# Performance work log

Measured on AMD Instinct MI355X. Metric: run time of the kernel, lower is better.

## Reference

```python
import jax, jax.numpy as jnp
import numpy as np

N_NODES = 50000
N_EDGES = 800000
NODE_DIM = 64
EDGE_DIM = 16
NUM_LAYERS = 2


def setup_inputs() -> dict:
    key = jax.random.key(0)
    ks = jax.random.split(key, 16)
    nd, ed = NODE_DIM, EDGE_DIM
    cin = 2 * nd + ed  # 144
    s = 0.05
    return {
        "x": jax.random.normal(ks[0], (N_NODES, nd), jnp.float32),
        "edge_index": jax.random.randint(ks[1], (2, N_EDGES), 0, N_NODES, jnp.int64),
        "edge_features": jax.random.normal(ks[2], (N_EDGES, ed), jnp.float32),
        "num_nodes": N_NODES,
        # shared SAGE conv params (one conv module reused every layer)
        "conv_W": jax.random.normal(ks[3], (nd + nd + ed, nd), jnp.float32) * s,
        "conv_b": jnp.zeros((nd,), jnp.float32),
        # edge-prediction MLP head: (2*nd+ed) -> 256 -> 128 -> 64 -> 1
        "W1": jax.random.normal(ks[4], (cin, 256), jnp.float32) * s,
        "b1": jnp.zeros((256,), jnp.float32),
        "W2": jax.random.normal(ks[5], (256, 128), jnp.float32) * s,
        "b2": jnp.zeros((128,), jnp.float32),
        "W3": jax.random.normal(ks[6], (128, 64), jnp.float32) * s,
        "b3": jnp.zeros((64,), jnp.float32),
        "W4": jax.random.normal(ks[7], (64, 1), jnp.float32) * s,
        "b4": jnp.zeros((1,), jnp.float32),
    }


def _sage_conv(x, src, dst, edge_features, conv_W, conv_b, num_nodes):
    # message: concat(source node feature, edge feature), mean-aggregated at dst
    msg = jnp.concatenate([x[src], edge_features], axis=-1)  # [E, nd+ed]
    agg = jax.ops.segment_sum(msg, dst, num_segments=num_nodes)
    cnt = jax.ops.segment_sum(jnp.ones((src.shape[0],), x.dtype), dst, num_segments=num_nodes)
    agg = agg / jnp.maximum(cnt, 1.0)[:, None]
    h = jnp.concatenate([x, agg], axis=-1)  # [N, 2*nd+ed]
    return h @ conv_W + conv_b  # [N, nd]


def reference(x, edge_index, edge_features, num_nodes,
              conv_W, conv_b, W1, b1, W2, b2, W3, b3, W4, b4):
    src = edge_index[0]
    dst = edge_index[1]
    h = x
    for _ in range(NUM_LAYERS):
        h = _sage_conv(h, src, dst, edge_features, conv_W, conv_b, num_nodes)
        h = jax.nn.relu(h)  # dropout is identity in eval mode
    # edge prediction head: gather endpoint embeddings + edge features -> MLP
    pair = jnp.concatenate([h[src], h[dst], edge_features], axis=-1)  # [E, 2*nd+ed]
    z = jax.nn.relu(pair @ W1 + b1)
    z = jax.nn.relu(z @ W2 + b2)
    z = jax.nn.relu(z @ W3 + b3)
    return z @ W4 + b4  # [E, 1]
```

## Files before the change

### kernel.cpp

```cpp
#include <hip/hip_runtime.h>

#define ND 64
#define ED 16
#define NN 50000
#define NE 800000
#define CIN 144
#define AGGD 80
#define TE 32

typedef __attribute__((ext_vector_type(8))) short short8;
typedef __attribute__((ext_vector_type(4))) float f32x4;
typedef __attribute__((ext_vector_type(4))) unsigned int uint4v;
typedef __attribute__((ext_vector_type(4))) unsigned short ushort4v;

union FragU { uint4v u; short8 s; };

__device__ __forceinline__ unsigned bf16rne(float v) {
  unsigned u = __float_as_uint(v);
  return (u + 0x7fffu + ((u >> 16) & 1u)) >> 16;
}


__global__ __launch_bounds__(256) void count_kernel(const int* __restrict__ dst,
                                                    int* __restrict__ dcnt) {
  int t = blockIdx.x * 256 + threadIdx.x;
  if (t < NE) atomicAdd(&dcnt[dst[t]], 1);
}

__global__ __launch_bounds__(1024) void scan_kernel(const int* __restrict__ dcnt,
                                                    int* __restrict__ base) {
  __shared__ int s[1024];
  __shared__ int carry;
  int t = threadIdx.x;
  if (t == 0) carry = 0;
  __syncthreads();
  for (int c = 0; c < (NN + 1023) / 1024; ++c) {
    int i = c * 1024 + t;
    int v = (i < NN) ? dcnt[i] : 0;
    s[t] = v;
    __syncthreads();
    #pragma unroll
    for (int d = 1; d < 1024; d <<= 1) {
      int add = (t >= d) ? s[t - d] : 0;
      __syncthreads();
      s[t] += add;
      __syncthreads();
    }
    if (i < NN) base[i] = carry + s[t] - v;
    int tot = s[1023];
    __syncthreads();
    if (t == 0) carry += tot;
    __syncthreads();
  }
}

__global__ __launch_bounds__(256) void place_kernel(const int* __restrict__ src,
                                                    const int* __restrict__ dst,
                                                    const int* __restrict__ base,
                                                    int* __restrict__ fill,
                                                    int* __restrict__ sidx,
                                                    int* __restrict__ eidx) {
  int e = blockIdx.x * 256 + threadIdx.x;
  if (e < NE) {
    int d = dst[e];
    int slot = base[d] + atomicAdd(&fill[d], 1);
    sidx[slot] = src[e];
    eidx[slot] = e;
  }
}

template<bool WITH_EF>
__global__ __launch_bounds__(256) void gather_kernel(const float* __restrict__ h,
                                                     const int* __restrict__ sidx,
                                                     const int* __restrict__ eidx,
                                                     const float* __restrict__ ef,
                                                     const int* __restrict__ base,
                                                     const int* __restrict__ dcnt,
                                                     float* __restrict__ agg) {
  int wid  = (blockIdx.x * 256 + threadIdx.x) >> 6;
  int lane = threadIdx.x & 63;
  if (wid >= NN) return;
  int b0 = base[wid], deg = dcnt[wid];
  float acc = 0.f;
  int k = 0;
  for (; k + 2 <= deg; k += 2) {
    int s0 = sidx[b0 + k], s1 = sidx[b0 + k + 1];
    float a = h[(size_t)s0 * ND + lane];
    float b = h[(size_t)s1 * ND + lane];
    acc += a + b;
  }
  if (k < deg) acc += h[(size_t)sidx[b0 + k] * ND + lane];
  agg[(size_t)wid * AGGD + lane] = acc;
  if (WITH_EF) {
    int sub = lane >> 4, f = lane & 15;
    float ae = 0.f;
    for (int kk = sub; kk < deg; kk += 4)
      ae += ef[(size_t)eidx[b0 + kk] * ED + f];
    ae += __shfl_down(ae, 32);
    ae += __shfl_down(ae, 16);
    if (lane < 16) agg[(size_t)wid * AGGD + ND + lane] = ae;
  }
}

__global__ __launch_bounds__(256) void node_kernel(const float* __restrict__ h,
                                                   const float* __restrict__ agg,
                                                   const int* __restrict__ dcnt,
                                                   const float* __restrict__ W,
                                                   const float* __restrict__ b,
                                                   float* __restrict__ hout) {
  __shared__ float in[4][CIN];
  int j  = threadIdx.x & 63;
  int nl = threadIdx.x >> 6;
  int n  = blockIdx.x * 4 + nl;
  float inv = 1.0f / fmaxf((float)dcnt[n], 1.0f);
  in[nl][j]      = h[(size_t)n * ND + j];
  in[nl][ND + j] = agg[(size_t)n * AGGD + j] * inv;
  if (j < ED) in[nl][2 * ND + j] = agg[(size_t)n * AGGD + ND + j] * inv;
  __syncthreads();
  float acc = b[j];
  #pragma unroll 4
  for (int i = 0; i < CIN; i++)
    acc = fmaf(in[nl][i], W[i * ND + j], acc);
  hout[(size_t)n * ND + j] = fmaxf(acc, 0.0f);
}

template<int K, int KP, int NO, bool LO>
__global__ __launch_bounds__(256) void prep_kernel(const float* __restrict__ W,
                                                   unsigned short* __restrict__ WT) {
  constexpr int KS = KP / 32;
  int idx = blockIdx.x * 256 + threadIdx.x;
  if (idx >= KP * NO) return;
  int i  = idx & 7;
  int lr = (idx >> 3) & 15;
  int lk = (idx >> 7) & 3;
  int rest = idx >> 9;
  int ks = rest % KS, ct = rest / KS;
  int k = ks * 32 + lk * 8 + i;
  int n = ct * 16 + lr;
  float wv = (k < K) ? W[k * NO + n] : 0.f;
  unsigned hi = bf16rne(wv);
  unsigned outb = hi;
  if (LO) {
    float lo = wv - __uint_as_float(hi << 16);
    outb = bf16rne(lo);
  }
  WT[idx] = (unsigned short)outb;
}

template<int KP, int NO, int SIN, int SOUT, int CTW, bool F32OUT>
__device__ __forceinline__ void mfma_layer(
    const unsigned short* __restrict__ zh, const unsigned short* __restrict__ zl,
    unsigned short* __restrict__ oh, unsigned short* __restrict__ ol,
    float* __restrict__ of,
    const unsigned short* __restrict__ WTh, const unsigned short* __restrict__ WTl,
    const float* __restrict__ bias, int w, int l) {
  constexpr int KS = KP / 32;
  const int lr = l & 15, lk = l >> 4;
  const int ct0 = w * CTW;
  const unsigned short* a0h = zh + lr * SIN + lk * 8;
  const unsigned short* a1h = a0h + 16 * SIN;
  const unsigned short* a0l = zl + lr * SIN + lk * 8;
  const unsigned short* a1l = a0l + 16 * SIN;
  const unsigned short* wth = WTh + (size_t)(ct0 * KS) * 512 + l * 8;
  const unsigned short* wtl = WTl + (size_t)(ct0 * KS) * 512 + l * 8;

  f32x4 acc[CTW][2];
  #pragma unroll
  for (int j = 0; j < CTW; ++j) {
    acc[j][0] = f32x4{0.f, 0.f, 0.f, 0.f};
    acc[j][1] = f32x4{0.f, 0.f, 0.f, 0.f};
  }

  FragU whf[CTW], wlf[CTW], nwh[CTW], nwl[CTW];
  #pragma unroll
  for (int j = 0; j < CTW; ++j) {
    whf[j].u = *(const uint4v*)(wth + j * KS * 512);
    wlf[j].u = *(const uint4v*)(wtl + j * KS * 512);
  }

  #pragma unroll
  for (int ks = 0; ks < KS; ++ks) {
    FragU A0h, A1h, A0l, A1l;
    A0h.s = *(const short8*)(a0h + ks * 32);
    A1h.s = *(const short8*)(a1h + ks * 32);
    A0l.s = *(const short8*)(a0l + ks * 32);
    A1l.s = *(const short8*)(a1l + ks * 32);
    if (ks + 1 < KS) {
      #pragma unroll
      for (int j = 0; j < CTW; ++j) {
        nwh[j].u = *(const uint4v*)(wth + (j * KS + ks + 1) * 512);
        nwl[j].u = *(const uint4v*)(wtl + (j * KS + ks + 1) * 512);
      }
    }
    #pragma unroll
    for (int j = 0; j < CTW; ++j) {
      acc[j][0] = __builtin_amdgcn_mfma_f32_16x16x32_bf16(A0h.s, whf[j].s, acc[j][0], 0, 0, 0);
      acc[j][1] = __builtin_amdgcn_mfma_f32_16x16x32_bf16(A1h.s, whf[j].s, acc[j][1], 0, 0, 0);
      acc[j][0] = __builtin_amdgcn_mfma_f32_16x16x32_bf16(A0l.s, whf[j].s, acc[j][0], 0, 0, 0);
      acc[j][1] = __builtin_amdgcn_mfma_f32_16x16x32_bf16(A1l.s, whf[j].s, acc[j][1], 0, 0, 0);
      acc[j][0] = __builtin_amdgcn_mfma_f32_16x16x32_bf16(A0h.s, wlf[j].s, acc[j][0], 0, 0, 0);
      acc[j][1] = __builtin_amdgcn_mfma_f32_16x16x32_bf16(A1h.s, wlf[j].s, acc[j][1], 0, 0, 0);
    }
    if (ks + 1 < KS) {
      #pragma unroll
      for (int j = 0; j < CTW; ++j) { whf[j] = nwh[j]; wlf[j] = nwl[j]; }
    }
  }

  #pragma unroll
  for (int j = 0; j < CTW; ++j) {
    const int col = (ct0 + j) * 16 + lr;
    const float bb = bias[col];
    #pragma unroll
    for (int rb = 0; rb < 2; ++rb) {
      #pragma unroll
      for (int q = 0; q < 4; ++q) {
        const int row = rb * 16 + lk * 4 + q;
        float v = fmaxf(acc[j][rb][q] + bb, 0.f);
        if (F32OUT) {
          of[row * SOUT + col] = v;
        } else {
          unsigned hu = bf16rne(v);
          oh[row * SOUT + col] = (unsigned short)hu;
          float lo = v - __uint_as_float(hu << 16);
          ol[row * SOUT + col] = (unsigned short)bf16rne(lo);
        }
      }
    }
  }
}

__global__ __launch_bounds__(256, 2) void head_kernel(
    const float* __restrict__ h,
    const int* __restrict__ src, const int* __restrict__ dst,
    const float* __restrict__ ef,
    const unsigned short* __restrict__ WTh1, const unsigned short* __restrict__ WTl1,
    const unsigned short* __restrict__ WTh2, const unsigned short* __restrict__ WTl2,
    const unsigned short* __restrict__ WTh3, const unsigned short* __restrict__ WTl3,
    const float* __restrict__ b1, const float* __restrict__ b2,
    const float* __restrict__ b3,
    const float* __restrict__ W4, const float* __restrict__ b4,
    float* __restrict__ out) {
  __shared__ __align__(16) unsigned short bufA[2 * 32 * 168];
  __shared__ __align__(16) unsigned short bufB[2 * 32 * 264];
  const int t = threadIdx.x;
  const int e0 = blockIdx.x * TE;
  const int w = t >> 6, l = t & 63;

  unsigned short* PH  = bufA;
  unsigned short* PL  = bufA + 32 * 168;
  unsigned short* Z1H = bufB;
  unsigned short* Z1L = bufB + 32 * 264;
  unsigned short* Z2H = bufA;
  unsigned short* Z2L = bufA + 32 * 136;
  float* Z3 = (float*)bufB;

  {
    int el = t & 31, q = t >> 5;
    int e = e0 + el;
    int s = src[e], d = dst[e];
    #pragma unroll
    for (int p5 = 0; p5 < 5; ++p5) {
      int qq = q + p5 * 8;
      float4 v = {0.f, 0.f, 0.f, 0.f};
      if (qq < 16)      v = ((const float4*)(h + (size_t)s * ND))[qq];
      else if (qq < 32) v = ((const float4*)(h + (size_t)d * ND))[qq - 16];
      else if (qq < 36) v = ((const float4*)(ef + (size_t)e * ED))[qq - 32];
      unsigned h0 = bf16rne(v.x), h1 = bf16rne(v.y),
               h2 = bf16rne(v.z), h3 = bf16rne(v.w);
      ushort4v hv = {(unsigned short)h0, (unsigned short)h1,
                     (unsigned short)h2, (unsigned short)h3};
      ushort4v lv = {(unsigned short)bf16rne(v.x - __uint_as_float(h0 << 16)),
                     (unsigned short)bf16rne(v.y - __uint_as_float(h1 << 16)),
                     (unsigned short)bf16rne(v.z - __uint_as_float(h2 << 16)),
                     (unsigned short)bf16rne(v.w - __uint_as_float(h3 << 16))};
      *(ushort4v*)(PH + el * 168 + qq * 4) = hv;
      *(ushort4v*)(PL + el * 168 + qq * 4) = lv;
    }
  }
  __syncthreads();
  mfma_layer<160, 256, 168, 264, 4, false>(PH, PL, Z1H, Z1L, nullptr,
                                           WTh1, WTl1, b1, w, l);
  __syncthreads();
  mfma_layer<256, 128, 264, 136, 2, false>(Z1H, Z1L, Z2H, Z2L, nullptr,
                                           WTh2, WTl2, b2, w, l);
  __syncthreads();
  mfma_layer<128, 64, 136, 68, 1, true>(Z2H, Z2L, nullptr, nullptr, Z3,
                                        WTh3, WTl3, b3, w, l);
  __syncthreads();
  if (t < TE) {
    const float* zr = Z3 + t * 68;
    float acc = b4[0];
    #pragma unroll
    for (int q = 0; q < 16; ++q) {
      float4 z  = *(const float4*)(zr + q * 4);
      float4 wv = *(const float4*)(W4 + q * 4);
      acc = fmaf(z.x, wv.x, acc); acc = fmaf(z.y, wv.y, acc);
      acc = fmaf(z.z, wv.z, acc); acc = fmaf(z.w, wv.w, acc);
    }
    out[e0 + t] = acc;
  }
}


extern "C" void kernel_launch(void* const* d_in, const int* in_sizes, int n_in,
                              void* d_out, int out_size, void* d_ws, size_t ws_size,
                              hipStream_t stream) {
  const float* x  = (const float*)d_in[0];
  const int*   ei = (const int*)d_in[1];
  const float* ef = (const float*)d_in[2];
  const float* cW = (const float*)d_in[4];
  const float* cb = (const float*)d_in[5];
  const float* W1 = (const float*)d_in[6];
  const float* b1 = (const float*)d_in[7];
  const float* W2 = (const float*)d_in[8];
  const float* b2 = (const float*)d_in[9];
  const float* W3 = (const float*)d_in[10];
  const float* b3 = (const float*)d_in[11];
  const float* W4 = (const float*)d_in[12];
  const float* b4 = (const float*)d_in[13];
  float* outp = (float*)d_out;

  const int* src = ei;
  const int* dst = ei + NE;

  float* h_a  = (float*)d_ws;
  float* h_b  = h_a + (size_t)NN * ND;
  float* agg  = h_b + (size_t)NN * ND;
  int*   dcnt = (int*)(agg + (size_t)NN * AGGD);
  int*   base = dcnt + NN;
  int*   fill = base + NN;
  int*   sidx = fill + NN;
  int*   eidx = sidx + NE;
  unsigned short* WTh1 =
      (unsigned short*)(((uintptr_t)(eidx + NE) + 63) & ~(uintptr_t)63);
  unsigned short* WTl1 = WTh1 + 160 * 256;
  unsigned short* WTh2 = WTl1 + 160 * 256;
  unsigned short* WTl2 = WTh2 + 256 * 128;
  unsigned short* WTh3 = WTl2 + 256 * 128;
  unsigned short* WTl3 = WTh3 + 128 * 64;

  prep_kernel<144, 160, 256, false><<<160, 256, 0, stream>>>(W1, WTh1);
  prep_kernel<144, 160, 256, true ><<<160, 256, 0, stream>>>(W1, WTl1);
  prep_kernel<256, 256, 128, false><<<128, 256, 0, stream>>>(W2, WTh2);
  prep_kernel<256, 256, 128, true ><<<128, 256, 0, stream>>>(W2, WTl2);
  prep_kernel<128, 128,  64, false><<< 32, 256, 0, stream>>>(W3, WTh3);
  prep_kernel<128, 128,  64, true ><<< 32, 256, 0, stream>>>(W3, WTl3);

  hipMemsetAsync(dcnt, 0, NN * sizeof(int), stream);
  hipMemsetAsync(fill, 0, NN * sizeof(int), stream);
  count_kernel<<<(NE + 255) / 256, 256, 0, stream>>>(dst, dcnt);
  scan_kernel<<<1, 1024, 0, stream>>>(dcnt, base);
  place_kernel<<<(NE + 255) / 256, 256, 0, stream>>>(src, dst, base, fill, sidx, eidx);

  gather_kernel<true><<<NN / 4, 256, 0, stream>>>(x, sidx, eidx, ef, base, dcnt, agg);
  node_kernel<<<NN / 4, 256, 0, stream>>>(x, agg, dcnt, cW, cb, h_a);

  gather_kernel<false><<<NN / 4, 256, 0, stream>>>(h_a, sidx, eidx, ef, base, dcnt, agg);
  node_kernel<<<NN / 4, 256, 0, stream>>>(h_a, agg, dcnt, cW, cb, h_b);

  head_kernel<<<NE / TE, 256, 0, stream>>>(h_b, src, dst, ef,
                                           WTh1, WTl1, WTh2, WTl2, WTh3, WTl3,
                                           b1, b2, b3, W4, b4, outp);
}
```

Baseline: 1.075 ms.

## Swizzle head LDS tiles into MFMA fragment layout, parallelize scan, merge prep kernels

Activation tiles in the head kernel are now stored in LDS already arranged in MFMA fragment order, so each lane reads its fragment contiguously. Bias is folded into the accumulator init, bf16 hi/lo splitting uses packed conversion, and shared memory is shrunk so occupancy can rise to three blocks per CU. Separately, the single-block serial scan becomes a three-kernel multi-block shuffle scan, and the six weight prep launches are merged into one. The intent is to cut LDS bank conflicts, conversion ALU work and launch or serial overhead, at the cost of more complex indexing.

```diff
diff --git a/kernel.cpp b/kernel.cpp
--- a/kernel.cpp
+++ b/kernel.cpp
@@ -1,4 +1,5 @@
 #include <hip/hip_runtime.h>
+#include <hip/hip_bf16.h>
 
 #define ND 64
 #define ED 16
@@ -7,6 +8,7 @@
 #define CIN 144
 #define AGGD 80
 #define TE 32
+#define NB 49
 
 typedef __attribute__((ext_vector_type(8))) short short8;
 typedef __attribute__((ext_vector_type(4))) float f32x4;
@@ -19,6 +21,11 @@
   unsigned u = __float_as_uint(v);
   return (u + 0x7fffu + ((u >> 16) & 1u)) >> 16;
 }
+__device__ __forceinline__ unsigned pk_bf16(float a, float b) {
+  __hip_bfloat162 h = __float22bfloat162_rn(float2{a, b});
+  unsigned r; __builtin_memcpy(&r, &h, 4);
+  return r;
+}
 
 
 __global__ __launch_bounds__(256) void count_kernel(const int* __restrict__ dst,
@@ -27,31 +34,54 @@
   if (t < NE) atomicAdd(&dcnt[dst[t]], 1);
 }
 
-__global__ __launch_bounds__(1024) void scan_kernel(const int* __restrict__ dcnt,
-                                                    int* __restrict__ base) {
-  __shared__ int s[1024];
-  __shared__ int carry;
+__global__ __launch_bounds__(1024) void scan1_kernel(const int* __restrict__ dcnt,
+                                                     int* __restrict__ base,
+                                                     int* __restrict__ bsum) {
+  __shared__ int ws[16];
+  int b = blockIdx.x, t = threadIdx.x;
+  int i = b * 1024 + t;
+  int v = (i < NN) ? dcnt[i] : 0;
+  int x = v;
+  int lane = t & 63;
+  #pragma unroll
+  for (int d = 1; d < 64; d <<= 1) {
+    int y = __shfl_up(x, d, 64);
+    if (lane >= d) x += y;
+  }
+  if (lane == 63) ws[t >> 6] = x;
+  __syncthreads();
+  if (t < 16) {
+    int y = ws[t];
+    #pragma unroll
+    for (int d = 1; d < 16; d <<= 1) {
+      int z = __shfl_up(y, d, 16);
+      if (t >= d) y += z;
+    }
+    ws[t] = y;
+  }
+  __syncthreads();
+  int woff = (t >= 64) ? ws[(t >> 6) - 1] : 0;
+  int incl = x + woff;
+  if (i < NN) base[i] = incl - v;
+  if (t == 1023) bsum[b] = incl;
+}
+
+__global__ __launch_bounds__(64) void scan2_kernel(int* __restrict__ bsum) {
   int t = threadIdx.x;
-  if (t == 0) carry = 0;
-  __syncthreads();
-  for (int c = 0; c < (NN + 1023) / 1024; ++c) {
-    int i = c * 1024 + t;
-    int v = (i < NN) ? dcnt[i] : 0;
-    s[t] = v;
-    __syncthreads();
-    #pragma unroll
-    for (int d = 1; d < 1024; d <<= 1) {
-      int add = (t >= d) ? s[t - d] : 0;
-      __syncthreads();
-      s[t] += add;
-      __syncthreads();
-    }
-    if (i < NN) base[i] = carry + s[t] - v;
-    int tot = s[1023];
-    __syncthreads();
-    if (t == 0) carry += tot;
-    __syncthreads();
-  }
+  int v = (t < NB) ? bsum[t] : 0;
+  int x = v;
+  #pragma unroll
+  for (int d = 1; d < 64; d <<= 1) {
+    int y = __shfl_up(x, d, 64);
+    if (t >= d) x += y;
+  }
+  if (t < NB) bsum[t] = x - v;
+}
+
+__global__ __launch_bounds__(256) void scan3_kernel(int* __restrict__ base,
+                                                    const int* __restrict__ bsum) {
+  int i = blockIdx.x * 256 + threadIdx.x;
+  if (i < NN) base[i] += bsum[i >> 10];
 }
 
 __global__ __launch_bounds__(256) void place_kernel(const int* __restrict__ src,
@@ -125,10 +155,11 @@
 }
 
 template<int K, int KP, int NO, bool LO>
-__global__ __launch_bounds__(256) void prep_kernel(const float* __restrict__ W,
-                                                   unsigned short* __restrict__ WT) {
+__device__ __forceinline__ void prep_body(const float* __restrict__ W,
+                                          unsigned short* __restrict__ WT,
+                                          int bx, int tx) {
   constexpr int KS = KP / 32;
-  int idx = blockIdx.x * 256 + threadIdx.x;
+  int idx = bx * 256 + tx;
   if (idx >= KP * NO) return;
   int i  = idx & 7;
   int lr = (idx >> 3) & 15;
@@ -147,7 +178,22 @@
   WT[idx] = (unsigned short)outb;
 }
 
-template<int KP, int NO, int SIN, int SOUT, int CTW, bool F32OUT>
+__global__ __launch_bounds__(256) void prep_all_kernel(
+    const float* __restrict__ W1, const float* __restrict__ W2,
+    const float* __restrict__ W3,
+    unsigned short* __restrict__ WTh1, unsigned short* __restrict__ WTl1,
+    unsigned short* __restrict__ WTh2, unsigned short* __restrict__ WTl2,
+    unsigned short* __restrict__ WTh3, unsigned short* __restrict__ WTl3) {
+  int bx = blockIdx.x, tx = threadIdx.x;
+  if      (bx < 160) prep_body<144, 160, 256, false>(W1, WTh1, bx, tx);
+  else if (bx < 320) prep_body<144, 160, 256, true >(W1, WTl1, bx - 160, tx);
+  else if (bx < 448) prep_body<256, 256, 128, false>(W2, WTh2, bx - 320, tx);
+  else if (bx < 576) prep_body<256, 256, 128, true >(W2, WTl2, bx - 448, tx);
+  else if (bx < 608) prep_body<128, 128,  64, false>(W3, WTh3, bx - 576, tx);
+  else               prep_body<128, 128,  64, true >(W3, WTl3, bx - 608, tx);
+}
+
+template<int KP, int NO, int CTW, int KSO, bool F32OUT>
 __device__ __forceinline__ void mfma_layer(
     const unsigned short* __restrict__ zh, const unsigned short* __restrict__ zl,
     unsigned short* __restrict__ oh, unsigned short* __restrict__ ol,
@@ -157,18 +203,17 @@
   constexpr int KS = KP / 32;
   const int lr = l & 15, lk = l >> 4;
   const int ct0 = w * CTW;
-  const unsigned short* a0h = zh + lr * SIN + lk * 8;
-  const unsigned short* a1h = a0h + 16 * SIN;
-  const unsigned short* a0l = zl + lr * SIN + lk * 8;
-  const unsigned short* a1l = a0l + 16 * SIN;
+  const unsigned short* ah = zh + l * 8;
+  const unsigned short* al = zl + l * 8;
   const unsigned short* wth = WTh + (size_t)(ct0 * KS) * 512 + l * 8;
   const unsigned short* wtl = WTl + (size_t)(ct0 * KS) * 512 + l * 8;
 
   f32x4 acc[CTW][2];
   #pragma unroll
   for (int j = 0; j < CTW; ++j) {
-    acc[j][0] = f32x4{0.f, 0.f, 0.f, 0.f};
-    acc[j][1] = f32x4{0.f, 0.f, 0.f, 0.f};
+    float bb = bias[(ct0 + j) * 16 + lr];
+    acc[j][0] = f32x4{bb, bb, bb, bb};
+    acc[j][1] = f32x4{bb, bb, bb, bb};
   }
 
   FragU whf[CTW], wlf[CTW], nwh[CTW], nwl[CTW];
@@ -181,10 +226,10 @@
   #pragma unroll
   for (int ks = 0; ks < KS; ++ks) {
     FragU A0h, A1h, A0l, A1l;
-    A0h.s = *(const short8*)(a0h + ks * 32);
-    A1h.s = *(const short8*)(a1h + ks * 32);
-    A0l.s = *(const short8*)(a0l + ks * 32);
-    A1l.s = *(const short8*)(a1l + ks * 32);
+    A0h.s = *(const short8*)(ah + ks * 512);
+    A1h.s = *(const short8*)(ah + (KS + ks) * 512);
+    A0l.s = *(const short8*)(al + ks * 512);
+    A1l.s = *(const short8*)(al + (KS + ks) * 512);
     if (ks + 1 < KS) {
       #pragma unroll
       for (int j = 0; j < CTW; ++j) {
@@ -209,28 +254,41 @@
 
   #pragma unroll
   for (int j = 0; j < CTW; ++j) {
-    const int col = (ct0 + j) * 16 + lr;
-    const float bb = bias[col];
+    const int col0 = (ct0 + j) * 16 + lr;
     #pragma unroll
     for (int rb = 0; rb < 2; ++rb) {
-      #pragma unroll
-      for (int q = 0; q < 4; ++q) {
-        const int row = rb * 16 + lk * 4 + q;
-        float v = fmaxf(acc[j][rb][q] + bb, 0.f);
-        if (F32OUT) {
-          of[row * SOUT + col] = v;
-        } else {
-          unsigned hu = bf16rne(v);
-          oh[row * SOUT + col] = (unsigned short)hu;
-          float lo = v - __uint_as_float(hu << 16);
-          ol[row * SOUT + col] = (unsigned short)bf16rne(lo);
-        }
+      float v0 = fmaxf(acc[j][rb][0], 0.f);
+      float v1 = fmaxf(acc[j][rb][1], 0.f);
+      float v2 = fmaxf(acc[j][rb][2], 0.f);
+      float v3 = fmaxf(acc[j][rb][3], 0.f);
+      if (F32OUT) {
+        const int r0 = rb * 16 + lk * 4;
+        of[(r0 + 0) * 68 + col0] = v0;
+        of[(r0 + 1) * 68 + col0] = v1;
+        of[(r0 + 2) * 68 + col0] = v2;
+        of[(r0 + 3) * 68 + col0] = v3;
+      } else {
+        unsigned uh01 = pk_bf16(v0, v1), uh23 = pk_bf16(v2, v3);
+        unsigned ul01 = pk_bf16(v0 - __uint_as_float(uh01 << 16),
+                                v1 - __uint_as_float(uh01 & 0xffff0000u));
+        unsigned ul23 = pk_bf16(v2 - __uint_as_float(uh23 << 16),
+                                v3 - __uint_as_float(uh23 & 0xffff0000u));
+        const int o = (rb * KSO + (col0 >> 5)) * 512 +
+                      ((col0 & 31) >> 3) * 128 + lk * 32 + (col0 & 7);
+        oh[o]      = (unsigned short)(uh01 & 0xffffu);
+        oh[o + 8]  = (unsigned short)(uh01 >> 16);
+        oh[o + 16] = (unsigned short)(uh23 & 0xffffu);
+        oh[o + 24] = (unsigned short)(uh23 >> 16);
+        ol[o]      = (unsigned short)(ul01 & 0xffffu);
+        ol[o + 8]  = (unsigned short)(ul01 >> 16);
+        ol[o + 16] = (unsigned short)(ul23 & 0xffffu);
+        ol[o + 24] = (unsigned short)(ul23 >> 16);
       }
     }
   }
 }
 
-__global__ __launch_bounds__(256, 2) void head_kernel(
+__global__ __launch_bounds__(256, 3) void head_kernel(
     const float* __restrict__ h,
     const int* __restrict__ src, const int* __restrict__ dst,
     const float* __restrict__ ef,
@@ -241,52 +299,54 @@
     const float* __restrict__ b3,
     const float* __restrict__ W4, const float* __restrict__ b4,
     float* __restrict__ out) {
-  __shared__ __align__(16) unsigned short bufA[2 * 32 * 168];
-  __shared__ __align__(16) unsigned short bufB[2 * 32 * 264];
+  __shared__ __align__(16) unsigned short S[26624];
+  unsigned short* PH  = S;
+  unsigned short* PL  = S + 5120;
+  unsigned short* Z1H = S + 10240;
+  unsigned short* Z1L = S + 18432;
+  unsigned short* Z2H = S;
+  unsigned short* Z2L = S + 4096;
+  float*          Z3  = (float*)(S + 8192);
+
   const int t = threadIdx.x;
   const int e0 = blockIdx.x * TE;
   const int w = t >> 6, l = t & 63;
 
-  unsigned short* PH  = bufA;
-  unsigned short* PL  = bufA + 32 * 168;
-  unsigned short* Z1H = bufB;
-  unsigned short* Z1L = bufB + 32 * 264;
-  unsigned short* Z2H = bufA;
-  unsigned short* Z2L = bufA + 32 * 136;
-  float* Z3 = (float*)bufB;
-
   {
-    int el = t & 31, q = t >> 5;
+    int el = t & 31, q8 = t >> 5;
+    int rb = el >> 4, lra = el & 15;
     int e = e0 + el;
     int s = src[e], d = dst[e];
     #pragma unroll
     for (int p5 = 0; p5 < 5; ++p5) {
-      int qq = q + p5 * 8;
+      int qq = q8 + p5 * 8;
       float4 v = {0.f, 0.f, 0.f, 0.f};
       if (qq < 16)      v = ((const float4*)(h + (size_t)s * ND))[qq];
       else if (qq < 32) v = ((const float4*)(h + (size_t)d * ND))[qq - 16];
       else if (qq < 36) v = ((const float4*)(ef + (size_t)e * ED))[qq - 32];
-      unsigned h0 = bf16rne(v.x), h1 = bf16rne(v.y),
-               h2 = bf16rne(v.z), h3 = bf16rne(v.w);
-      ushort4v hv = {(unsigned short)h0, (unsigned short)h1,
-                     (unsigned short)h2, (unsigned short)h3};
-      ushort4v lv = {(unsigned short)bf16rne(v.x - __uint_as_float(h0 << 16)),
-                     (unsigned short)bf16rne(v.y - __uint_as_float(h1 << 16)),
-                     (unsigned short)bf16rne(v.z - __uint_as_float(h2 << 16)),
-                     (unsigned short)bf16rne(v.w - __uint_as_float(h3 << 16))};
-      *(ushort4v*)(PH + el * 168 + qq * 4) = hv;
-      *(ushort4v*)(PL + el * 168 + qq * 4) = lv;
-    }
-  }
-  __syncthreads();
-  mfma_layer<160, 256, 168, 264, 4, false>(PH, PL, Z1H, Z1L, nullptr,
-                                           WTh1, WTl1, b1, w, l);
-  __syncthreads();
-  mfma_layer<256, 128, 264, 136, 2, false>(Z1H, Z1L, Z2H, Z2L, nullptr,
-                                           WTh2, WTl2, b2, w, l);
-  __syncthreads();
-  mfma_layer<128, 64, 136, 68, 1, true>(Z2H, Z2L, nullptr, nullptr, Z3,
-                                        WTh3, WTl3, b3, w, l);
+      unsigned uh01 = pk_bf16(v.x, v.y), uh23 = pk_bf16(v.z, v.w);
+      unsigned ul01 = pk_bf16(v.x - __uint_as_float(uh01 << 16),
+                              v.y - __uint_as_float(uh01 & 0xffff0000u));
+      unsigned ul23 = pk_bf16(v.z - __uint_as_float(uh23 << 16),
+                              v.w - __uint_as_float(uh23 & 0xffff0000u));
+      int idx = (rb * 5 + (qq >> 3)) * 512 + ((qq & 7) >> 1) * 128 +
+                lra * 8 + (qq & 1) * 4;
+      *(ushort4v*)(PH + idx) = ushort4v{(unsigned short)(uh01 & 0xffffu),
+                                        (unsigned short)(uh01 >> 16),
+                                        (unsigned short)(uh23 & 0xffffu),
+                                        (unsigned short)(uh23 >> 16)};
+      *(ushort4v*)(PL + idx) = ushort4v{(unsigned short)(ul01 & 0xffffu),
+                                        (unsigned short)(ul01 >> 16),
+                                        (unsigned short)(ul23 & 0xffffu),
+                                        (unsigned short)(ul23 >> 16)};
+    }
+  }
+  __syncthreads();
+  mfma_layer<160, 256, 4, 8, false>(PH, PL, Z1H, Z1L, nullptr, WTh1, WTl1, b1, w, l);
+  __syncthreads();
+  mfma_layer<256, 128, 2, 4, false>(Z1H, Z1L, Z2H, Z2L, nullptr, WTh2, WTl2, b2, w, l);
+  __syncthreads();
+  mfma_layer<128, 64, 1, 1, true>(Z2H, Z2L, nullptr, nullptr, Z3, WTh3, WTl3, b3, w, l);
   __syncthreads();
   if (t < TE) {
     const float* zr = Z3 + t * 68;
@@ -332,25 +392,24 @@
   int*   fill = base + NN;
   int*   sidx = fill + NN;
   int*   eidx = sidx + NE;
+  int*   bsum = eidx + NE;
   unsigned short* WTh1 =
-      (unsigned short*)(((uintptr_t)(eidx + NE) + 63) & ~(uintptr_t)63);
+      (unsigned short*)(((uintptr_t)(bsum + NB) + 63) & ~(uintptr_t)63);
   unsigned short* WTl1 = WTh1 + 160 * 256;
   unsigned short* WTh2 = WTl1 + 160 * 256;
   unsigned short* WTl2 = WTh2 + 256 * 128;
   unsigned short* WTh3 = WTl2 + 256 * 128;
   unsigned short* WTl3 = WTh3 + 128 * 64;
 
-  prep_kernel<144, 160, 256, false><<<160, 256, 0, stream>>>(W1, WTh1);
-  prep_kernel<144, 160, 256, true ><<<160, 256, 0, stream>>>(W1, WTl1);
-  prep_kernel<256, 256, 128, false><<<128, 256, 0, stream>>>(W2, WTh2);
-  prep_kernel<256, 256, 128, true ><<<128, 256, 0, stream>>>(W2, WTl2);
-  prep_kernel<128, 128,  64, false><<< 32, 256, 0, stream>>>(W3, WTh3);
-  prep_kernel<128, 128,  64, true ><<< 32, 256, 0, stream>>>(W3, WTl3);
+  prep_all_kernel<<<640, 256, 0, stream>>>(W1, W2, W3, WTh1, WTl1,
+                                           WTh2, WTl2, WTh3, WTl3);
 
   hipMemsetAsync(dcnt, 0, NN * sizeof(int), stream);
   hipMemsetAsync(fill, 0, NN * sizeof(int), stream);
   count_kernel<<<(NE + 255) / 256, 256, 0, stream>>>(dst, dcnt);
-  scan_kernel<<<1, 1024, 0, stream>>>(dcnt, base);
+  scan1_kernel<<<NB, 1024, 0, stream>>>(dcnt, base, bsum);
+  scan2_kernel<<<1, 64, 0, stream>>>(bsum);
+  scan3_kernel<<<(NN + 255) / 256, 256, 0, stream>>>(base, bsum);
   place_kernel<<<(NE + 255) / 256, 256, 0, stream>>>(src, dst, base, fill, sidx, eidx);
 
   gather_kernel<true><<<NN / 4, 256, 0, stream>>>(x, sidx, eidx, ef, base, dcnt, agg);
```

Result: faster. 891.7 us (-17.0%).
